# Kernel optimization log

Hardware: AMD Instinct MI355X
Metric: run time of the kernel (lower is better)

Reference implementation:

```python
import jax, jax.numpy as jnp
import numpy as np
import math

EPS = 1e-5

def make_coords(H, W):
    # Faithful port of generate_coordinates (batch-independent; channels 8,9 stay zero).
    cy = H / 2.0 - 0.5
    cx = W / 2.0 - 0.5
    gx, gy = np.meshgrid(np.arange(H, dtype=np.float32), np.arange(W, dtype=np.float32), indexing='ij')
    two_pi = 2.0 * math.pi
    theta = np.arctan2(gy - cx, gx - cy) % two_pi
    theta = np.round(10000.0 * theta) / 10000.0
    coords = np.zeros((H, W, 18), dtype=np.float32)
    adds = [(1, 1), (1, 0), (1, -1), (0, 1), None, (0, -1), (-1, 1), (-1, 0), (-1, -1)]
    for k, add in enumerate(adds):
        if add is None:
            continue  # center tap offset left at zero (as in source)
        n = k if k < 4 else k - 1
        a = theta + n * (two_pi / 8.0)
        coords[:, :, 2 * k] = np.cos(a) + add[0]
        coords[:, :, 2 * k + 1] = np.sin(a) + add[1]
    return jnp.asarray(coords)

def bilinear_sample(x, py, px):
    # x: [B,C,H,W]; py/px: [H,W] sample coords; zero outside boundaries (torchvision semantics).
    H, W = x.shape[2], x.shape[3]
    y0f = jnp.floor(py); x0f = jnp.floor(px)
    wy1 = py - y0f; wy0 = 1.0 - wy1
    wx1 = px - x0f; wx0 = 1.0 - wx1
    def gather(yf, xf):
        valid = ((yf >= 0) & (yf < H) & (xf >= 0) & (xf < W)).astype(x.dtype)
        yi = jnp.clip(yf, 0, H - 1).astype(jnp.int32)
        xi = jnp.clip(xf, 0, W - 1).astype(jnp.int32)
        return x[:, :, yi, xi] * valid  # [B,C,H,W]
    return (gather(y0f, x0f) * (wy0 * wx0) + gather(y0f, x0f + 1) * (wy0 * wx1)
            + gather(y0f + 1, x0f) * (wy1 * wx0) + gather(y0f + 1, x0f + 1) * (wy1 * wx1))

def deform_conv(x, coords, weight, pad=1):
    # x: [B,Cin,H,W]; coords: [H,W,18] with (dy,dx) pairs per 3x3 tap; weight: [Cout,Cin,3,3]; no bias.
    B, C, H, W = x.shape
    ys = jnp.arange(H, dtype=x.dtype)[:, None]
    xs = jnp.arange(W, dtype=x.dtype)[None, :]
    out = jnp.zeros((B, weight.shape[0], H, W), x.dtype)
    for k in range(9):  # fixed 3x3 taps
        kh, kw = k // 3, k % 3
        py = ys - pad + kh + coords[..., 2 * k]
        px = xs - pad + kw + coords[..., 2 * k + 1]
        samp = bilinear_sample(x, py, px)
        out = out + jnp.einsum('bchw,oc->bohw', samp, weight[:, :, kh, kw])
    return out

def bn_relu(x, gamma, beta):
    # BatchNorm2d in training mode (batch statistics, biased variance) + ReLU.
    mu = x.mean(axis=(0, 2, 3), keepdims=True)
    var = ((x - mu) ** 2).mean(axis=(0, 2, 3), keepdims=True)
    xn = (x - mu) * jax.lax.rsqrt(var + EPS)
    return jax.nn.relu(xn * gamma[None, :, None, None] + beta[None, :, None, None])

def maxpool2(x):
    B, C, H, W = x.shape
    return x.reshape(B, C, H // 2, 2, W // 2, 2).max(axis=(3, 5))

def setup_inputs() -> dict:
    key = jax.random.key(0)
    ks = jax.random.split(key, 16)
    B = 1024
    def conv_w(k, co, ci):
        return jax.random.normal(k, (co, ci, 3, 3), jnp.float32) * (1.0 / np.sqrt(ci * 9))
    inp = {
        'x': jax.random.normal(ks[0], (B, 1, 32, 32), jnp.float32),
        'w11': conv_w(ks[1], 32, 1),  'g11': jnp.ones(32),  'b11': jnp.zeros(32),
        'w12': conv_w(ks[2], 32, 32), 'g12': jnp.ones(32),  'b12': jnp.zeros(32),
        'w21': conv_w(ks[3], 64, 32), 'g21': jnp.ones(64),  'b21': jnp.zeros(64),
        'w22': conv_w(ks[4], 64, 64), 'g22': jnp.ones(64),  'b22': jnp.zeros(64),
        'w31': conv_w(ks[5], 128, 64),  'g31': jnp.ones(128), 'b31': jnp.zeros(128),
        'w32': conv_w(ks[6], 128, 128), 'g32': jnp.ones(128), 'b32': jnp.zeros(128),
        'fcw': jax.random.normal(ks[7], (10, 128), jnp.float32) * (1.0 / np.sqrt(128)),
        'fcb': jnp.zeros(10),
        'c32': make_coords(32, 32),
        'c16': make_coords(16, 16),
        'c8': make_coords(8, 8),
    }
    return inp

def reference(x, w11, g11, b11, w12, g12, b12, w21, g21, b21, w22, g22, b22,
              w31, g31, b31, w32, g32, b32, fcw, fcb, c32, c16, c8):
    x = bn_relu(deform_conv(x, c32, w11), g11, b11)
    x = bn_relu(deform_conv(x, c32, w12), g12, b12)
    x = maxpool2(x)                      # [B,32,16,16]
    x = bn_relu(deform_conv(x, c16, w21), g21, b21)
    x = bn_relu(deform_conv(x, c16, w22), g22, b22)
    x = maxpool2(x)                      # [B,64,8,8]
    x = bn_relu(deform_conv(x, c8, w31), g31, b31)
    x = bn_relu(deform_conv(x, c8, w32), g32, b32)
    x = x.mean(axis=(2, 3))              # AvgPool2d(8) over full 8x8 -> [B,128]
    return x @ fcw.T + fcb               # [B,10]
```

## Files before the change

### kernel.cpp

```cpp
#include <hip/hip_runtime.h>
#include <math.h>


#define BATCH 1024
typedef unsigned short u16;
typedef unsigned int uint;
typedef __attribute__((ext_vector_type(8))) short short8;
typedef __attribute__((ext_vector_type(4))) float f32x4;
typedef __attribute__((ext_vector_type(2))) float f32x2;

__device__ __forceinline__ float b2f(u16 v) {
    return __uint_as_float(((uint)v) << 16);
}
__device__ __forceinline__ float4 b2f4(ushort4 v) {
    return make_float4(b2f(v.x), b2f(v.y), b2f(v.z), b2f(v.w));
}
__device__ __forceinline__ u16 f2b(float f) {
    uint u = __float_as_uint(f);
    return (u16)((u + 0x7FFFu + ((u >> 16) & 1u)) >> 16);
}
__device__ __forceinline__ float ldf(const void* p, long long i, int isbf) {
    return isbf ? b2f(((const u16*)p)[i]) : ((const float*)p)[i];
}
__device__ __forceinline__ f32x2 upk(uint u) {
    f32x2 r;
    r.x = __uint_as_float(u << 16);
    r.y = __uint_as_float(u & 0xFFFF0000u);
    return r;
}

struct Ptrs { const void* p[24]; int sz[24]; };

__global__ __launch_bounds__(256) void probe_dtype(Ptrs P, int* __restrict__ flags)
{
    int t = blockIdx.x;
    bool ones = (t == 2 || t == 5 || t == 8 || t == 11 || t == 14 || t == 17);
    bool inh  = (t == 3 || t == 6 || t == 9 || t == 12 || t == 15 || t == 18 || t == 20);
    if (inh) return;
    const u16* q = (const u16*)P.p[t];
    if (ones) {
        if (threadIdx.x == 0) {
            uint w0 = *(const uint*)q;
            flags[t] = (w0 == 0x3F803F80u) ? 1 : 0;
        }
        return;
    }
    int n = P.sz[t]; if (n > 4096) n = 4096;
    __shared__ int cnt;
    if (threadIdx.x == 0) cnt = 0;
    __syncthreads();
    int local = 0;
    for (int i = threadIdx.x; i < n; i += 256) {
        uint e = (q[i] >> 7) & 0xFFu;
        if (!(e == 0u || (e >= 100u && e <= 140u))) local++;
    }
    atomicAdd(&cnt, local);
    __syncthreads();
    if (threadIdx.x == 0) flags[t] = (cnt * 8 > n) ? 0 : 1;
}

__global__ void fixup_flags(int* __restrict__ flags)
{
    if (threadIdx.x == 0) {
        flags[3] = flags[2];  flags[6] = flags[5];  flags[9] = flags[8];
        flags[12] = flags[11]; flags[15] = flags[14]; flags[18] = flags[17];
        flags[20] = flags[19];
    }
}

__device__ void table_body(const void* coords, int H, int W,
                           int* tIdx, float* tW, int fcd, int i)
{
    int HW = H * W;
    if (i >= HW * 9) return;
    int p = i / 9, k = i % 9;
    int h = p / W, w = p % W;
    int kh = k / 3, kw = k % 3;
    float py = (float)(h - 1 + kh) + ldf(coords, p * 18 + 2 * k, fcd);
    float px = (float)(w - 1 + kw) + ldf(coords, p * 18 + 2 * k + 1, fcd);
    float y0f = floorf(py), x0f = floorf(px);
    float wy1 = py - y0f, wy0 = 1.0f - wy1;
    float wx1 = px - x0f, wx0 = 1.0f - wx1;
    int y0 = (int)y0f, x0 = (int)x0f;
#pragma unroll
    for (int j = 0; j < 4; ++j) {
        int dy = j >> 1, dx = j & 1;
        int yy = y0 + dy, xx = x0 + dx;
        bool valid = (yy >= 0) && (yy < H) && (xx >= 0) && (xx < W);
        int yc = min(max(yy, 0), H - 1);
        int xc = min(max(xx, 0), W - 1);
        tIdx[i * 4 + j] = yc * W + xc;
        tW[i * 4 + j] = valid ? (dy ? wy1 : wy0) * (dx ? wx1 : wx0) : 0.0f;
    }
}

__global__ __launch_bounds__(256) void build_tables(
    const void* c32, const void* c16, const void* c8,
    int* tI32, float* tW32, int* tI16, float* tW16, int* tI8, float* tW8,
    const int* __restrict__ flags)
{
    int b = blockIdx.x, t = threadIdx.x;
    if (b < 36)      table_body(c32, 32, 32, tI32, tW32, flags[21], b * 256 + t);
    else if (b < 45) table_body(c16, 16, 16, tI16, tW16, flags[22], (b - 36) * 256 + t);
    else             table_body(c8, 8, 8, tI8, tW8, flags[23], (b - 45) * 256 + t);
}

__global__ __launch_bounds__(256) void transpose_in(
    const void* __restrict__ x, u16* __restrict__ X0, const int* __restrict__ flags)
{
    int fx = flags[0];
    int p = blockIdx.x;
    int t = threadIdx.x;
    ushort4 v;
    v.x = f2b(ldf(x, (long long)(4 * t + 0) * 1024 + p, fx));
    v.y = f2b(ldf(x, (long long)(4 * t + 1) * 1024 + p, fx));
    v.z = f2b(ldf(x, (long long)(4 * t + 2) * 1024 + p, fx));
    v.w = f2b(ldf(x, (long long)(4 * t + 3) * 1024 + p, fx));
    ((ushort4*)(X0 + (size_t)p * BATCH))[t] = v;
}

__device__ void wb_body(const void* W, u16* Wb, int Cout, int Cin, int fw, int i)
{
    int c8 = i & 7;
    int r = i >> 3;
    int m = r % Cout;
    int r2 = r / Cout;
    int noct = Cin >> 3;
    int oc = r2 % noct;
    int k = r2 / noct;
    int c = oc * 8 + c8;
    Wb[i] = f2b(ldf(W, (long long)m * Cin * 9 + c * 9 + k, fw));
}

__global__ __launch_bounds__(256) void prep_all(
    const void* w11, const void* w12, const void* w21, const void* w22,
    const void* w31, const void* w32,
    float* w11p, u16* wb12, u16* wb21, u16* wb22, u16* wb31, u16* wb32,
    const int* __restrict__ flags)
{
    int i = blockIdx.x * 256 + threadIdx.x;
    if (i < 288) {
        int o = i / 9, k = i % 9;
        w11p[k * 32 + o] = ldf(w11, i, flags[1]);
    } else if (i < 9504)   wb_body(w12, wb12, 32, 32, flags[4], i - 288);
    else if (i < 27936)    wb_body(w21, wb21, 64, 32, flags[7], i - 9504);
    else if (i < 64800)    wb_body(w22, wb22, 64, 64, flags[10], i - 27936);
    else if (i < 138528)   wb_body(w31, wb31, 128, 64, flags[13], i - 64800);
    else if (i < 285984)   wb_body(w32, wb32, 128, 128, flags[16], i - 138528);
}

__global__ __launch_bounds__(256) void conv_l11(
    const u16* __restrict__ X0, const float* __restrict__ W2,
    u16* __restrict__ Y, const int* __restrict__ tIdx, const float* __restrict__ tW)
{
    const int id = blockIdx.x;
    const int p = id >> 1;
    const int oBase = (id & 1) * 16;
    const int b4 = threadIdx.x;
    const ushort4* Xu = (const ushort4*)X0;

    float4 acc[16];
#pragma unroll
    for (int o = 0; o < 16; ++o) acc[o] = make_float4(0.f, 0.f, 0.f, 0.f);

#pragma unroll
    for (int k = 0; k < 9; ++k) {
        float4 s = make_float4(0.f, 0.f, 0.f, 0.f);
#pragma unroll
        for (int j = 0; j < 4; ++j) {
            float wgt = tW[p * 36 + k * 4 + j];
            int pix = tIdx[p * 36 + k * 4 + j];
            float4 v = b2f4(Xu[pix * 256 + b4]);
            s.x = fmaf(wgt, v.x, s.x); s.y = fmaf(wgt, v.y, s.y);
            s.z = fmaf(wgt, v.z, s.z); s.w = fmaf(wgt, v.w, s.w);
        }
#pragma unroll
        for (int o = 0; o < 16; ++o) {
            float wv = W2[k * 32 + oBase + o];
            acc[o].x = fmaf(wv, s.x, acc[o].x); acc[o].y = fmaf(wv, s.y, acc[o].y);
            acc[o].z = fmaf(wv, s.z, acc[o].z); acc[o].w = fmaf(wv, s.w, acc[o].w);
        }
    }
#pragma unroll
    for (int bb = 0; bb < 4; ++bb) {
        u16 h[16];
#pragma unroll
        for (int o = 0; o < 16; ++o) h[o] = f2b((&acc[o].x)[bb]);
        uint4 pk;
        pk.x = (uint)h[0] | ((uint)h[1] << 16);
        pk.y = (uint)h[2] | ((uint)h[3] << 16);
        pk.z = (uint)h[4] | ((uint)h[5] << 16);
        pk.w = (uint)h[6] | ((uint)h[7] << 16);
        uint4 pk2;
        pk2.x = (uint)h[8] | ((uint)h[9] << 16);
        pk2.y = (uint)h[10] | ((uint)h[11] << 16);
        pk2.z = (uint)h[12] | ((uint)h[13] << 16);
        pk2.w = (uint)h[14] | ((uint)h[15] << 16);
        size_t base = ((size_t)p * 1024 + 4 * b4 + bb) * 32 + oBase;
        *(uint4*)(Y + base) = pk;
        *(uint4*)(Y + base + 8) = pk2;
    }
}

template<int MF, int NF>
__global__ __launch_bounds__(256) void conv_mfma(
    const u16* __restrict__ X, const u16* __restrict__ Wb,
    u16* __restrict__ Y,
    const int* __restrict__ tIdx, const float* __restrict__ tW,
    int Cin, int Cout, int HW, int pshift)
{
    const int tid = threadIdx.x;
    const int wid = tid >> 6;
    const int lane = tid & 63;
    const int quad = lane >> 4;
    const int l16 = lane & 15;

    const int pper = HW >> 3;
    const int xcd = blockIdx.x & 7;
    const int lid = blockIdx.x >> 3;
    const int p = xcd * pper + (lid & (pper - 1));
    const int yq = lid >> pshift;

    const int nb = yq * (4 * NF * 16);
    const int wn = wid * (NF * 16);

    const int noct = Cin >> 3;
    const size_t pixstride = (size_t)1024 * Cin;

    int roff[NF];
#pragma unroll
    for (int nf = 0; nf < NF; ++nf)
        roff[nf] = (nb + wn + nf * 16 + l16) * Cin + quad * 8;

    f32x4 acc[MF][NF];
#pragma unroll
    for (int mf = 0; mf < MF; ++mf)
#pragma unroll
        for (int nf = 0; nf < NF; ++nf)
            acc[mf][nf] = (f32x4){0.f, 0.f, 0.f, 0.f};

    const int nc = Cin >> 5;
    for (int k = 0; k < 9; ++k) {
        int pix[4]; f32x2 ww[4];
#pragma unroll
        for (int j = 0; j < 4; ++j) {
            pix[j] = __builtin_amdgcn_readfirstlane(tIdx[p * 36 + k * 4 + j]);
            float w = __uint_as_float(__builtin_amdgcn_readfirstlane(
                __float_as_uint(tW[p * 36 + k * 4 + j])));
            ww[j].x = w; ww[j].y = w;
        }
        const u16* xb0 = X + (size_t)pix[0] * pixstride;
        const u16* xb1 = X + (size_t)pix[1] * pixstride;
        const u16* xb2 = X + (size_t)pix[2] * pixstride;
        const u16* xb3 = X + (size_t)pix[3] * pixstride;

        for (int cc = 0; cc < nc; ++cc) {
            const int coff = cc << 5;
            short8 bf[NF];
#pragma unroll
            for (int nf = 0; nf < NF; ++nf) {
                int ro = roff[nf] + coff;
                uint4 v0 = *(const uint4*)(xb0 + ro);
                uint4 v1 = *(const uint4*)(xb1 + ro);
                uint4 v2 = *(const uint4*)(xb2 + ro);
                uint4 v3 = *(const uint4*)(xb3 + ro);
                const uint* a0 = &v0.x; const uint* a1 = &v1.x;
                const uint* a2 = &v2.x; const uint* a3 = &v3.x;
                union { short8 s; uint4 u; } cvt;
                uint o[4];
#pragma unroll
                for (int i = 0; i < 4; ++i) {
                    f32x2 a = upk(a0[i]) * ww[0];
                    a = upk(a1[i]) * ww[1] + a;
                    a = upk(a2[i]) * ww[2] + a;
                    a = upk(a3[i]) * ww[3] + a;
                    o[i] = __builtin_amdgcn_perm(
                        __float_as_uint(a.y) + 0x8000u,
                        __float_as_uint(a.x) + 0x8000u, 0x07060302u);
                }
                cvt.u.x = o[0]; cvt.u.y = o[1]; cvt.u.z = o[2]; cvt.u.w = o[3];
                bf[nf] = cvt.s;
            }
            const u16* wk = Wb + ((size_t)(k * noct + (cc << 2) + quad) * Cout + l16) * 8;
#pragma unroll
            for (int mf = 0; mf < MF; ++mf) {
                const short8 af = *(const short8*)(wk + (size_t)mf * 16 * 8);
#pragma unroll
                for (int nf = 0; nf < NF; ++nf)
                    acc[mf][nf] = __builtin_amdgcn_mfma_f32_16x16x32_bf16(
                        af, bf[nf], acc[mf][nf], 0, 0, 0);
            }
        }
    }

#pragma unroll
    for (int mf = 0; mf < MF; ++mf) {
        int cout0 = mf * 16 + quad * 4;
#pragma unroll
        for (int nf = 0; nf < NF; ++nf) {
            int b = nb + wn + nf * 16 + l16;
            ushort4 pk;
            pk.x = f2b(acc[mf][nf][0]);
            pk.y = f2b(acc[mf][nf][1]);
            pk.z = f2b(acc[mf][nf][2]);
            pk.w = f2b(acc[mf][nf][3]);
            *(ushort4*)(Y + ((size_t)p * 1024 + b) * Cout + cout0) = pk;
        }
    }
}

__global__ __launch_bounds__(256) void bn_stats2(
    const u16* __restrict__ Y, float* __restrict__ stats, int Cin, long long NPB)
{
    const int stride = Cin >> 3;
    const int RPI = 256 / stride;
    const int t = threadIdx.x;
    const int cg = t % stride;
    const int r = t / stride;
    const int lane = t & 63;
    const int wid = t >> 6;

    float s[8], q[8];
#pragma unroll
    for (int j = 0; j < 8; ++j) { s[j] = 0.f; q[j] = 0.f; }

    for (long long row0 = (long long)blockIdx.x * RPI; row0 < NPB;
         row0 += (long long)gridDim.x * RPI) {
        long long row = row0 + r;
        if (row >= NPB) continue;
        uint4 v = *(const uint4*)(Y + row * Cin + cg * 8);
        uint ua[4] = {v.x, v.y, v.z, v.w};
#pragma unroll
        for (int jj = 0; jj < 4; ++jj) {
            float lo = __uint_as_float(ua[jj] << 16);
            float hi = __uint_as_float(ua[jj] & 0xFFFF0000u);
            s[2 * jj] += lo;     q[2 * jj] += lo * lo;
            s[2 * jj + 1] += hi; q[2 * jj + 1] += hi * hi;
        }
    }
    for (int off = 32; off >= stride; off >>= 1) {
#pragma unroll
        for (int j = 0; j < 8; ++j) {
            s[j] += __shfl_down(s[j], off);
            q[j] += __shfl_down(q[j], off);
        }
    }
    __shared__ float rs[4][128], rq[4][128];
    if (lane < stride) {
#pragma unroll
        for (int j = 0; j < 8; ++j) {
            rs[wid][lane * 8 + j] = s[j];
            rq[wid][lane * 8 + j] = q[j];
        }
    }
    __syncthreads();
    if (t < Cin) {
        float S = rs[0][t] + rs[1][t] + rs[2][t] + rs[3][t];
        float Q = rq[0][t] + rq[1][t] + rq[2][t] + rq[3][t];
        atomicAdd(&stats[2 * t], S);
        atomicAdd(&stats[2 * t + 1], Q);
    }
}

__global__ __launch_bounds__(256) void bn_apply2(
    u16* __restrict__ Y, const float* __restrict__ stats,
    const void* __restrict__ gamma, const void* __restrict__ beta,
    int Cin, float invN, long long total8,
    const int* __restrict__ flags, int gslot, int bslot)
{
    __shared__ float sSC[128], sSH[128];
    int fg = flags[gslot], fb = flags[bslot];
    if (threadIdx.x < Cin) {
        int c = threadIdx.x;
        float mean = stats[2 * c] * invN;
        float var = stats[2 * c + 1] * invN - mean * mean;
        float sc = ldf(gamma, c, fg) * rsqrtf(var + 1e-5f);
        sSC[c] = sc;
        sSH[c] = ldf(beta, c, fb) - mean * sc;
    }
    __syncthreads();
    const int stride = Cin >> 3;
    for (long long i = (long long)blockIdx.x * 256 + threadIdx.x; i < total8;
         i += (long long)gridDim.x * 256) {
        int cg = (int)(i % stride);
        uint4* ptr = (uint4*)(Y + i * 8);
        uint4 v = *ptr;
        uint ua[4] = {v.x, v.y, v.z, v.w};
#pragma unroll
        for (int jj = 0; jj < 4; ++jj) {
            int c = cg * 8 + 2 * jj;
            float lo = __uint_as_float(ua[jj] << 16);
            float hi = __uint_as_float(ua[jj] & 0xFFFF0000u);
            lo = fmaxf(fmaf(lo, sSC[c], sSH[c]), 0.f);
            hi = fmaxf(fmaf(hi, sSC[c + 1], sSH[c + 1]), 0.f);
            ua[jj] = ((uint)f2b(hi) << 16) | (uint)f2b(lo);
        }
        v.x = ua[0]; v.y = ua[1]; v.z = ua[2]; v.w = ua[3];
        *ptr = v;
    }
}

__global__ __launch_bounds__(256) void pool_bn(
    const u16* __restrict__ A, u16* __restrict__ P,
    const float* __restrict__ stats,
    const void* __restrict__ gamma, const void* __restrict__ beta,
    const int* __restrict__ flags, int gslot, int bslot,
    int H2, int W2, int C, float invN, long long total)
{
    __shared__ float sSC[128], sSH[128];
    if (threadIdx.x < C) {
        int c = threadIdx.x;
        float mean = stats[2 * c] * invN;
        float var = stats[2 * c + 1] * invN - mean * mean;
        float sc = ldf(gamma, c, flags[gslot]) * rsqrtf(var + 1e-5f);
        sSC[c] = sc;
        sSH[c] = ldf(beta, c, flags[bslot]) - mean * sc;
    }
    __syncthreads();
    long long i = (long long)blockIdx.x * 256 + threadIdx.x;
    if (i >= total) return;
    int cgn = C >> 3;
    int cg = (int)(i % cgn);
    long long row = i / cgn;
    int b = (int)(row & 1023);
    int p2 = (int)(row >> 10);
    int h2 = p2 / W2, w2 = p2 % W2;
    int W = 2 * W2;
    int p00 = (2 * h2) * W + 2 * w2;
    const u16* base = A + (size_t)cg * 8;
    uint4 va = *(const uint4*)(base + ((size_t)(p00)*1024 + b) * C);
    uint4 vb = *(const uint4*)(base + ((size_t)(p00 + 1) * 1024 + b) * C);
    uint4 vd = *(const uint4*)(base + ((size_t)(p00 + W) * 1024 + b) * C);
    uint4 ve = *(const uint4*)(base + ((size_t)(p00 + W + 1) * 1024 + b) * C);
    uint ra[4] = {va.x, va.y, va.z, va.w};
    uint rb[4] = {vb.x, vb.y, vb.z, vb.w};
    uint rd[4] = {vd.x, vd.y, vd.z, vd.w};
    uint re[4] = {ve.x, ve.y, ve.z, ve.w};
    uint ro[4];
#pragma unroll
    for (int j = 0; j < 4; ++j) {
        int c = cg * 8 + 2 * j;
        float lo = fmaxf(fmaxf(__uint_as_float(ra[j] << 16), __uint_as_float(rb[j] << 16)),
                         fmaxf(__uint_as_float(rd[j] << 16), __uint_as_float(re[j] << 16)));
        float hi = fmaxf(fmaxf(__uint_as_float(ra[j] & 0xFFFF0000u), __uint_as_float(rb[j] & 0xFFFF0000u)),
                         fmaxf(__uint_as_float(rd[j] & 0xFFFF0000u), __uint_as_float(re[j] & 0xFFFF0000u)));
        lo = fmaxf(fmaf(lo, sSC[c], sSH[c]), 0.f);
        hi = fmaxf(fmaf(hi, sSC[c + 1], sSH[c + 1]), 0.f);
        ro[j] = ((uint)f2b(hi) << 16) | (uint)f2b(lo);
    }
    uint4 m; m.x = ro[0]; m.y = ro[1]; m.z = ro[2]; m.w = ro[3];
    *(uint4*)(P + ((size_t)p2 * 1024 + b) * C + cg * 8) = m;
}

__global__ __launch_bounds__(256) void avg_bn(
    const u16* __restrict__ A, float* __restrict__ M,
    const float* __restrict__ stats,
    const void* __restrict__ gamma, const void* __restrict__ beta,
    const int* __restrict__ flags, int gslot, int bslot, float invN)
{
    __shared__ float sSC[128], sSH[128];
    if (threadIdx.x < 128) {
        int c = threadIdx.x;
        float mean = stats[2 * c] * invN;
        float var = stats[2 * c + 1] * invN - mean * mean;
        float sc = ldf(gamma, c, flags[gslot]) * rsqrtf(var + 1e-5f);
        sSC[c] = sc;
        sSH[c] = ldf(beta, c, flags[bslot]) - mean * sc;
    }
    __syncthreads();
    int i = blockIdx.x * 256 + threadIdx.x;
    int b = i >> 4, cg = i & 15;
    float s[8];
#pragma unroll
    for (int j = 0; j < 8; ++j) s[j] = 0.f;
    for (int p = 0; p < 64; ++p) {
        uint4 v = *(const uint4*)(A + ((size_t)p * 1024 + b) * 128 + cg * 8);
        uint ua[4] = {v.x, v.y, v.z, v.w};
#pragma unroll
        for (int jj = 0; jj < 4; ++jj) {
            int c = cg * 8 + 2 * jj;
            float lo = __uint_as_float(ua[jj] << 16);
            float hi = __uint_as_float(ua[jj] & 0xFFFF0000u);
            s[2 * jj] += fmaxf(fmaf(lo, sSC[c], sSH[c]), 0.f);
            s[2 * jj + 1] += fmaxf(fmaf(hi, sSC[c + 1], sSH[c + 1]), 0.f);
        }
    }
#pragma unroll
    for (int j = 0; j < 8; ++j) M[(size_t)b * 128 + cg * 8 + j] = s[j] * (1.0f / 64.0f);
}

__global__ __launch_bounds__(256) void fc_naive(
    const float* __restrict__ M, const void* __restrict__ fcw,
    const void* __restrict__ fcb, float* __restrict__ out, int total,
    const int* __restrict__ flags)
{
    int fw = flags[19], fb = flags[20];
    int i = blockIdx.x * 256 + threadIdx.x;
    if (i >= total) return;
    int o = i % 10, b = i / 10;
    float acc = ldf(fcb, o, fb);
    const float* Mb = M + (size_t)b * 128;
    for (int c = 0; c < 128; ++c) acc = fmaf(Mb[c], ldf(fcw, (size_t)o * 128 + c, fw), acc);
    out[i] = acc;
}

__global__ __launch_bounds__(256) void sentinel_k(float* out, int n, float v) {
    int i = blockIdx.x * 256 + threadIdx.x;
    if (i < n) out[i] = v;
}

extern "C" void kernel_launch(void* const* d_in, const int* in_sizes, int n_in,
                              void* d_out, int out_size, void* d_ws, size_t ws_size,
                              hipStream_t stream) {
    float* out = (float*)d_out;

    static const int exp_sizes[24] = {
        1024 * 1024,
        288, 32, 32,   9216, 32, 32,   18432, 64, 64,   36864, 64, 64,
        73728, 128, 128,   147456, 128, 128,
        1280, 10,   18432, 4608, 1152
    };
    float bad = 0.0f;
    if (n_in != 24) bad = 1000.0f;
    else {
        for (int i = 0; i < 24; ++i)
            if (in_sizes[i] != exp_sizes[i]) { bad = 2000.0f + 16.0f * i; break; }
    }
    if (bad != 0.0f) {
        sentinel_k<<<(out_size + 255) / 256, 256, 0, stream>>>(out, out_size, bad);
        return;
    }

    Ptrs P;
    for (int i = 0; i < 24; ++i) { P.p[i] = d_in[i]; P.sz[i] = in_sizes[i]; }

    char* wsb = (char*)d_ws;
    size_t off = 0;
    auto take = [&](size_t bytes) -> void* {
        void* pp = wsb + off;
        off += (bytes + 255) & ~(size_t)255;
        return pp;
    };
    int*   flags = (int*)  take(32 * 4);
    float* stats = (float*)take(6 * 256 * 4);
    int*   tI32  = (int*)  take(1024 * 36 * 4);
    float* tW32  = (float*)take(1024 * 36 * 4);
    int*   tI16  = (int*)  take(256 * 36 * 4);
    float* tW16  = (float*)take(256 * 36 * 4);
    int*   tI8   = (int*)  take(64 * 36 * 4);
    float* tW8   = (float*)take(64 * 36 * 4);
    float* w11p  = (float*)take(32 * 9 * 4);
    u16*   wb12  = (u16*)  take(32 * 32 * 9 * 2);
    u16*   wb21  = (u16*)  take(64 * 32 * 9 * 2);
    u16*   wb22  = (u16*)  take(64 * 64 * 9 * 2);
    u16*   wb31  = (u16*)  take(128 * 64 * 9 * 2);
    u16*   wb32  = (u16*)  take(128 * 128 * 9 * 2);
    u16*   X0    = (u16*)  take((size_t)1024 * BATCH * 2);
    float* M     = (float*)take((size_t)BATCH * 128 * 4);
    u16*   bufA  = (u16*)  take((size_t)32 * 1024 * BATCH * 2);
    u16*   bufB  = (u16*)  take((size_t)32 * 1024 * BATCH * 2);

    if (ws_size < off) {
        sentinel_k<<<(out_size + 255) / 256, 256, 0, stream>>>(out, out_size, 12345.0f);
        return;
    }

    probe_dtype<<<24, 256, 0, stream>>>(P, flags);
    fixup_flags<<<1, 64, 0, stream>>>(flags);
    hipMemsetAsync(stats, 0, 6 * 256 * 4, stream);
    build_tables<<<48, 256, 0, stream>>>(d_in[21], d_in[22], d_in[23],
                                         tI32, tW32, tI16, tW16, tI8, tW8, flags);
    transpose_in<<<1024, 256, 0, stream>>>(d_in[0], X0, flags);
    prep_all<<<1118, 256, 0, stream>>>(d_in[1], d_in[4], d_in[7], d_in[10], d_in[13], d_in[16],
                                       w11p, wb12, wb21, wb22, wb31, wb32, flags);

    float* st0 = stats + 0 * 256;
    float* st1 = stats + 1 * 256;
    float* st2 = stats + 2 * 256;
    float* st3 = stats + 3 * 256;
    float* st4 = stats + 4 * 256;
    float* st5 = stats + 5 * 256;

    conv_l11<<<2048, 256, 0, stream>>>(X0, w11p, bufA, tI32, tW32);
    bn_stats2<<<256, 256, 0, stream>>>(bufA, st0, 32, 1048576LL);
    bn_apply2<<<2048, 256, 0, stream>>>(bufA, st0, d_in[2], d_in[3], 32,
                                        1.0f / 1048576.0f, 4194304LL, flags, 2, 3);
    conv_mfma<2, 4><<<4096, 256, 0, stream>>>(bufA, wb12, bufB, tI32, tW32, 32, 32, 1024, 7);
    bn_stats2<<<256, 256, 0, stream>>>(bufB, st1, 32, 1048576LL);
    pool_bn<<<4096, 256, 0, stream>>>(bufB, bufA, st1, d_in[5], d_in[6], flags, 5, 6,
                                      16, 16, 32, 1.0f / 1048576.0f, 1048576LL);
    conv_mfma<4, 4><<<1024, 256, 0, stream>>>(bufA, wb21, bufB, tI16, tW16, 32, 64, 256, 5);
    bn_stats2<<<256, 256, 0, stream>>>(bufB, st2, 64, 262144LL);
    bn_apply2<<<2048, 256, 0, stream>>>(bufB, st2, d_in[8], d_in[9], 64,
                                        1.0f / 262144.0f, 2097152LL, flags, 8, 9);
    conv_mfma<4, 4><<<1024, 256, 0, stream>>>(bufB, wb22, bufA, tI16, tW16, 64, 64, 256, 5);
    bn_stats2<<<256, 256, 0, stream>>>(bufA, st3, 64, 262144LL);
    pool_bn<<<2048, 256, 0, stream>>>(bufA, bufB, st3, d_in[11], d_in[12], flags, 11, 12,
                                      8, 8, 64, 1.0f / 262144.0f, 524288LL);
    conv_mfma<8, 2><<<512, 256, 0, stream>>>(bufB, wb31, bufA, tI8, tW8, 64, 128, 64, 3);
    bn_stats2<<<256, 256, 0, stream>>>(bufA, st4, 128, 65536LL);
    bn_apply2<<<2048, 256, 0, stream>>>(bufA, st4, d_in[14], d_in[15], 128,
                                        1.0f / 65536.0f, 1048576LL, flags, 14, 15);
    conv_mfma<8, 2><<<512, 256, 0, stream>>>(bufA, wb32, bufB, tI8, tW8, 128, 128, 64, 3);
    bn_stats2<<<256, 256, 0, stream>>>(bufB, st5, 128, 65536LL);
    avg_bn<<<64, 256, 0, stream>>>(bufB, M, st5, d_in[17], d_in[18], flags, 17, 18,
                                   1.0f / 65536.0f);
    fc_naive<<<40, 256, 0, stream>>>(M, d_in[19], d_in[20], out, 10240, flags);
}
```

Baseline: 945.1 us.

## Fuse BN+ReLU into deformable conv input gather and drop bn_apply passes

Removes the three standalone bn_apply2 passes and applies batch-norm scale/shift plus ReLU inside conv_mfma to each gathered bilinear tap before interpolation. This saves a full read-modify-write of the activation tensor per layer. The conv loop order is swapped to channel-chunk outer, tap inner, so per-channel scale/shift are loaded once per chunk. NF is halved with grid doubled for layers 2-3 to raise parallelism. Normalization is now recomputed four times per sample per tap, which adds ALU work in the gather.

```diff
diff --git a/kernel.cpp b/kernel.cpp
--- a/kernel.cpp
+++ b/kernel.cpp
@@ -202,13 +202,29 @@
     }
 }
 
-template<int MF, int NF>
+template<int MF, int NF, int BNORM>
 __global__ __launch_bounds__(256) void conv_mfma(
     const u16* __restrict__ X, const u16* __restrict__ Wb,
     u16* __restrict__ Y,
     const int* __restrict__ tIdx, const float* __restrict__ tW,
-    int Cin, int Cout, int HW, int pshift)
-{
+    int Cin, int Cout, int HW, int pshift,
+    const float* __restrict__ stats, const void* __restrict__ gamma,
+    const void* __restrict__ beta, const int* __restrict__ flags,
+    int gslot, int bslot, float invN)
+{
+    __shared__ float sSC[128], sSH[128];
+    if (BNORM) {
+        if (threadIdx.x < Cin) {
+            int c = threadIdx.x;
+            float mean = stats[2 * c] * invN;
+            float var = stats[2 * c + 1] * invN - mean * mean;
+            float sc = ldf(gamma, c, flags[gslot]) * rsqrtf(var + 1e-5f);
+            sSC[c] = sc;
+            sSH[c] = ldf(beta, c, flags[bslot]) - mean * sc;
+        }
+        __syncthreads();
+    }
+
     const int tid = threadIdx.x;
     const int wid = tid >> 6;
     const int lane = tid & 63;
@@ -240,22 +256,31 @@
             acc[mf][nf] = (f32x4){0.f, 0.f, 0.f, 0.f};
 
     const int nc = Cin >> 5;
-    for (int k = 0; k < 9; ++k) {
-        int pix[4]; f32x2 ww[4];
-#pragma unroll
-        for (int j = 0; j < 4; ++j) {
-            pix[j] = __builtin_amdgcn_readfirstlane(tIdx[p * 36 + k * 4 + j]);
-            float w = __uint_as_float(__builtin_amdgcn_readfirstlane(
-                __float_as_uint(tW[p * 36 + k * 4 + j])));
-            ww[j].x = w; ww[j].y = w;
-        }
-        const u16* xb0 = X + (size_t)pix[0] * pixstride;
-        const u16* xb1 = X + (size_t)pix[1] * pixstride;
-        const u16* xb2 = X + (size_t)pix[2] * pixstride;
-        const u16* xb3 = X + (size_t)pix[3] * pixstride;
-
-        for (int cc = 0; cc < nc; ++cc) {
-            const int coff = cc << 5;
+    for (int cc = 0; cc < nc; ++cc) {
+        const int coff = cc << 5;
+        f32x2 sc2[4], sh2[4];
+        if (BNORM) {
+            int c0 = coff + quad * 8;
+#pragma unroll
+            for (int i = 0; i < 4; ++i) {
+                sc2[i] = *(const f32x2*)(sSC + c0 + 2 * i);
+                sh2[i] = *(const f32x2*)(sSH + c0 + 2 * i);
+            }
+        }
+        for (int k = 0; k < 9; ++k) {
+            int pix[4]; f32x2 ww[4];
+#pragma unroll
+            for (int j = 0; j < 4; ++j) {
+                pix[j] = __builtin_amdgcn_readfirstlane(tIdx[p * 36 + k * 4 + j]);
+                float w = __uint_as_float(__builtin_amdgcn_readfirstlane(
+                    __float_as_uint(tW[p * 36 + k * 4 + j])));
+                ww[j].x = w; ww[j].y = w;
+            }
+            const u16* xb0 = X + (size_t)pix[0] * pixstride;
+            const u16* xb1 = X + (size_t)pix[1] * pixstride;
+            const u16* xb2 = X + (size_t)pix[2] * pixstride;
+            const u16* xb3 = X + (size_t)pix[3] * pixstride;
+
             short8 bf[NF];
 #pragma unroll
             for (int nf = 0; nf < NF; ++nf) {
@@ -270,10 +295,22 @@
                 uint o[4];
 #pragma unroll
                 for (int i = 0; i < 4; ++i) {
-                    f32x2 a = upk(a0[i]) * ww[0];
-                    a = upk(a1[i]) * ww[1] + a;
-                    a = upk(a2[i]) * ww[2] + a;
-                    a = upk(a3[i]) * ww[3] + a;
+                    f32x2 t0 = upk(a0[i]), t1 = upk(a1[i]);
+                    f32x2 t2 = upk(a2[i]), t3 = upk(a3[i]);
+                    if (BNORM) {
+                        t0 = t0 * sc2[i] + sh2[i];
+                        t1 = t1 * sc2[i] + sh2[i];
+                        t2 = t2 * sc2[i] + sh2[i];
+                        t3 = t3 * sc2[i] + sh2[i];
+                        t0.x = fmaxf(t0.x, 0.f); t0.y = fmaxf(t0.y, 0.f);
+                        t1.x = fmaxf(t1.x, 0.f); t1.y = fmaxf(t1.y, 0.f);
+                        t2.x = fmaxf(t2.x, 0.f); t2.y = fmaxf(t2.y, 0.f);
+                        t3.x = fmaxf(t3.x, 0.f); t3.y = fmaxf(t3.y, 0.f);
+                    }
+                    f32x2 a = t0 * ww[0];
+                    a = t1 * ww[1] + a;
+                    a = t2 * ww[2] + a;
+                    a = t3 * ww[3] + a;
                     o[i] = __builtin_amdgcn_perm(
                         __float_as_uint(a.y) + 0x8000u,
                         __float_as_uint(a.x) + 0x8000u, 0x07060302u);
@@ -359,44 +396,6 @@
         float Q = rq[0][t] + rq[1][t] + rq[2][t] + rq[3][t];
         atomicAdd(&stats[2 * t], S);
         atomicAdd(&stats[2 * t + 1], Q);
-    }
-}
-
-__global__ __launch_bounds__(256) void bn_apply2(
-    u16* __restrict__ Y, const float* __restrict__ stats,
-    const void* __restrict__ gamma, const void* __restrict__ beta,
-    int Cin, float invN, long long total8,
-    const int* __restrict__ flags, int gslot, int bslot)
-{
-    __shared__ float sSC[128], sSH[128];
-    int fg = flags[gslot], fb = flags[bslot];
-    if (threadIdx.x < Cin) {
-        int c = threadIdx.x;
-        float mean = stats[2 * c] * invN;
-        float var = stats[2 * c + 1] * invN - mean * mean;
-        float sc = ldf(gamma, c, fg) * rsqrtf(var + 1e-5f);
-        sSC[c] = sc;
-        sSH[c] = ldf(beta, c, fb) - mean * sc;
-    }
-    __syncthreads();
-    const int stride = Cin >> 3;
-    for (long long i = (long long)blockIdx.x * 256 + threadIdx.x; i < total8;
-         i += (long long)gridDim.x * 256) {
-        int cg = (int)(i % stride);
-        uint4* ptr = (uint4*)(Y + i * 8);
-        uint4 v = *ptr;
-        uint ua[4] = {v.x, v.y, v.z, v.w};
-#pragma unroll
-        for (int jj = 0; jj < 4; ++jj) {
-            int c = cg * 8 + 2 * jj;
-            float lo = __uint_as_float(ua[jj] << 16);
-            float hi = __uint_as_float(ua[jj] & 0xFFFF0000u);
-            lo = fmaxf(fmaf(lo, sSC[c], sSH[c]), 0.f);
-            hi = fmaxf(fmaf(hi, sSC[c + 1], sSH[c + 1]), 0.f);
-            ua[jj] = ((uint)f2b(hi) << 16) | (uint)f2b(lo);
-        }
-        v.x = ua[0]; v.y = ua[1]; v.z = ua[2]; v.w = ua[3];
-        *ptr = v;
     }
 }
 
@@ -583,25 +582,24 @@
 
     conv_l11<<<2048, 256, 0, stream>>>(X0, w11p, bufA, tI32, tW32);
     bn_stats2<<<256, 256, 0, stream>>>(bufA, st0, 32, 1048576LL);
-    bn_apply2<<<2048, 256, 0, stream>>>(bufA, st0, d_in[2], d_in[3], 32,
-                                        1.0f / 1048576.0f, 4194304LL, flags, 2, 3);
-    conv_mfma<2, 4><<<4096, 256, 0, stream>>>(bufA, wb12, bufB, tI32, tW32, 32, 32, 1024, 7);
+    conv_mfma<2, 4, 1><<<4096, 256, 0, stream>>>(bufA, wb12, bufB, tI32, tW32, 32, 32, 1024, 7,
+                                                 st0, d_in[2], d_in[3], flags, 2, 3, 1.0f / 1048576.0f);
     bn_stats2<<<256, 256, 0, stream>>>(bufB, st1, 32, 1048576LL);
     pool_bn<<<4096, 256, 0, stream>>>(bufB, bufA, st1, d_in[5], d_in[6], flags, 5, 6,
                                       16, 16, 32, 1.0f / 1048576.0f, 1048576LL);
-    conv_mfma<4, 4><<<1024, 256, 0, stream>>>(bufA, wb21, bufB, tI16, tW16, 32, 64, 256, 5);
+    conv_mfma<4, 2, 0><<<2048, 256, 0, stream>>>(bufA, wb21, bufB, tI16, tW16, 32, 64, 256, 5,
+                                                 st0, d_in[2], d_in[3], flags, 2, 3, 0.f);
     bn_stats2<<<256, 256, 0, stream>>>(bufB, st2, 64, 262144LL);
-    bn_apply2<<<2048, 256, 0, stream>>>(bufB, st2, d_in[8], d_in[9], 64,
-                                        1.0f / 262144.0f, 2097152LL, flags, 8, 9);
-    conv_mfma<4, 4><<<1024, 256, 0, stream>>>(bufB, wb22, bufA, tI16, tW16, 64, 64, 256, 5);
+    conv_mfma<4, 2, 1><<<2048, 256, 0, stream>>>(bufB, wb22, bufA, tI16, tW16, 64, 64, 256, 5,
+                                                 st2, d_in[8], d_in[9], flags, 8, 9, 1.0f / 262144.0f);
     bn_stats2<<<256, 256, 0, stream>>>(bufA, st3, 64, 262144LL);
     pool_bn<<<2048, 256, 0, stream>>>(bufA, bufB, st3, d_in[11], d_in[12], flags, 11, 12,
                                       8, 8, 64, 1.0f / 262144.0f, 524288LL);
-    conv_mfma<8, 2><<<512, 256, 0, stream>>>(bufB, wb31, bufA, tI8, tW8, 64, 128, 64, 3);
+    conv_mfma<8, 1, 0><<<1024, 256, 0, stream>>>(bufB, wb31, bufA, tI8, tW8, 64, 128, 64, 3,
+                                                 st0, d_in[2], d_in[3], flags, 2, 3, 0.f);
     bn_stats2<<<256, 256, 0, stream>>>(bufA, st4, 128, 65536LL);
-    bn_apply2<<<2048, 256, 0, stream>>>(bufA, st4, d_in[14], d_in[15], 128,
-                                        1.0f / 65536.0f, 1048576LL, flags, 14, 15);
-    conv_mfma<8, 2><<<512, 256, 0, stream>>>(bufA, wb32, bufB, tI8, tW8, 128, 128, 64, 3);
+    conv_mfma<8, 1, 1><<<1024, 256, 0, stream>>>(bufA, wb32, bufB, tI8, tW8, 128, 128, 64, 3,
+                                                 st4, d_in[14], d_in[15], flags, 14, 15, 1.0f / 65536.0f);
     bn_stats2<<<256, 256, 0, stream>>>(bufB, st5, 128, 65536LL);
     avg_bn<<<64, 256, 0, stream>>>(bufB, M, st5, d_in[17], d_in[18], flags, 17, 18,
                                    1.0f / 65536.0f);
```

Measured after the change: 879.2 us. -7.0%, faster.

## Fold bilinear tap weights into per-position conv weights instead of blending activations

Applied to the files above, without the earlier changes.

Precomputes, in chunks of output positions, effective bf16 weights equal to each conv weight times its bilinear tap weight, so the MFMA kernel streams the 36 raw gathered pixels directly as B operands. This removes the per-element unpack/FMA/repack blending of four neighbours before each MFMA, at the cost of four times more MFMA work, extra prep kernels and launches per chunk, and a large per-position weight buffer in workspace. Tile shapes change for the later layers, and tap tables are staged in shared memory, including in the first-layer kernel. Rounding changes because products are rounded to bf16 before accumulation.

```diff
diff --git a/kernel.cpp b/kernel.cpp
--- a/kernel.cpp
+++ b/kernel.cpp
@@ -149,12 +149,49 @@
     else if (i < 285984)   wb_body(w32, wb32, 128, 128, flags[16], i - 138528);
 }
 
+__global__ __launch_bounds__(256) void prep_weff(
+    const u16* __restrict__ Wb, const float* __restrict__ tW,
+    u16* __restrict__ Weff, int Cout, int noct, int p0, long long total8)
+{
+    long long j = (long long)blockIdx.x * 256 + threadIdx.x;
+    if (j >= total8) return;
+    long long r = j;
+    int m = (int)(r % Cout); r /= Cout;
+    int oc = (int)(r % noct); r /= noct;
+    int kj = (int)(r % 36); r /= 36;
+    int pl = (int)r;
+    int k = kj >> 2;
+    float w = tW[(size_t)(p0 + pl) * 36 + kj];
+    union { short8 s; uint4 u; } in, outv;
+    in.s = *(const short8*)(Wb + ((size_t)(k * noct + oc) * Cout + m) * 8);
+    uint a[4] = {in.u.x, in.u.y, in.u.z, in.u.w};
+    f32x2 w2; w2.x = w; w2.y = w;
+    uint o[4];
+#pragma unroll
+    for (int i = 0; i < 4; ++i) {
+        f32x2 t = upk(a[i]) * w2;
+        o[i] = __builtin_amdgcn_perm(
+            __float_as_uint(t.y) + 0x8000u,
+            __float_as_uint(t.x) + 0x8000u, 0x07060302u);
+    }
+    outv.u.x = o[0]; outv.u.y = o[1]; outv.u.z = o[2]; outv.u.w = o[3];
+    *(short8*)(Weff + j * 8) = outv.s;
+}
+
 __global__ __launch_bounds__(256) void conv_l11(
     const u16* __restrict__ X0, const float* __restrict__ W2,
     u16* __restrict__ Y, const int* __restrict__ tIdx, const float* __restrict__ tW)
 {
+    __shared__ int sIdx[36];
+    __shared__ float sWt[36];
     const int id = blockIdx.x;
     const int p = id >> 1;
+    if (threadIdx.x < 36) {
+        sIdx[threadIdx.x] = tIdx[p * 36 + threadIdx.x];
+        sWt[threadIdx.x] = tW[p * 36 + threadIdx.x];
+    }
+    __syncthreads();
+
     const int oBase = (id & 1) * 16;
     const int b4 = threadIdx.x;
     const ushort4* Xu = (const ushort4*)X0;
@@ -168,8 +205,8 @@
         float4 s = make_float4(0.f, 0.f, 0.f, 0.f);
 #pragma unroll
         for (int j = 0; j < 4; ++j) {
-            float wgt = tW[p * 36 + k * 4 + j];
-            int pix = tIdx[p * 36 + k * 4 + j];
+            float wgt = sWt[k * 4 + j];
+            int pix = sIdx[k * 4 + j];
             float4 v = b2f4(Xu[pix * 256 + b4]);
             s.x = fmaf(wgt, v.x, s.x); s.y = fmaf(wgt, v.y, s.y);
             s.z = fmaf(wgt, v.z, s.z); s.w = fmaf(wgt, v.w, s.w);
@@ -203,24 +240,27 @@
 }
 
 template<int MF, int NF>
-__global__ __launch_bounds__(256) void conv_mfma(
-    const u16* __restrict__ X, const u16* __restrict__ Wb,
-    u16* __restrict__ Y,
-    const int* __restrict__ tIdx, const float* __restrict__ tW,
-    int Cin, int Cout, int HW, int pshift)
-{
+__global__ __launch_bounds__(256) void conv_mfma2(
+    const u16* __restrict__ X, const u16* __restrict__ Weff,
+    u16* __restrict__ Y, const int* __restrict__ tIdx,
+    int Cin, int Cout, int p0, int pper)
+{
+    __shared__ int sIdx[36];
+    const int xcd = blockIdx.x & 7;
+    const int lid = blockIdx.x >> 3;
+    const int pl = xcd * pper + (lid % pper);
+    const int yq = lid / pper;
+    const int p = p0 + pl;
+
+    if (threadIdx.x < 36) sIdx[threadIdx.x] = tIdx[p * 36 + threadIdx.x];
+    __syncthreads();
+
     const int tid = threadIdx.x;
     const int wid = tid >> 6;
     const int lane = tid & 63;
     const int quad = lane >> 4;
     const int l16 = lane & 15;
 
-    const int pper = HW >> 3;
-    const int xcd = blockIdx.x & 7;
-    const int lid = blockIdx.x >> 3;
-    const int p = xcd * pper + (lid & (pper - 1));
-    const int yq = lid >> pshift;
-
     const int nb = yq * (4 * NF * 16);
     const int wn = wid * (NF * 16);
 
@@ -240,48 +280,17 @@
             acc[mf][nf] = (f32x4){0.f, 0.f, 0.f, 0.f};
 
     const int nc = Cin >> 5;
-    for (int k = 0; k < 9; ++k) {
-        int pix[4]; f32x2 ww[4];
-#pragma unroll
-        for (int j = 0; j < 4; ++j) {
-            pix[j] = __builtin_amdgcn_readfirstlane(tIdx[p * 36 + k * 4 + j]);
-            float w = __uint_as_float(__builtin_amdgcn_readfirstlane(
-                __float_as_uint(tW[p * 36 + k * 4 + j])));
-            ww[j].x = w; ww[j].y = w;
-        }
-        const u16* xb0 = X + (size_t)pix[0] * pixstride;
-        const u16* xb1 = X + (size_t)pix[1] * pixstride;
-        const u16* xb2 = X + (size_t)pix[2] * pixstride;
-        const u16* xb3 = X + (size_t)pix[3] * pixstride;
-
-        for (int cc = 0; cc < nc; ++cc) {
-            const int coff = cc << 5;
+    for (int cc = 0; cc < nc; ++cc) {
+        const int coff = cc << 5;
+        for (int kj = 0; kj < 36; ++kj) {
+            int pix = __builtin_amdgcn_readfirstlane(sIdx[kj]);
+            const u16* xb = X + (size_t)pix * pixstride + coff;
             short8 bf[NF];
 #pragma unroll
-            for (int nf = 0; nf < NF; ++nf) {
-                int ro = roff[nf] + coff;
-                uint4 v0 = *(const uint4*)(xb0 + ro);
-                uint4 v1 = *(const uint4*)(xb1 + ro);
-                uint4 v2 = *(const uint4*)(xb2 + ro);
-                uint4 v3 = *(const uint4*)(xb3 + ro);
-                const uint* a0 = &v0.x; const uint* a1 = &v1.x;
-                const uint* a2 = &v2.x; const uint* a3 = &v3.x;
-                union { short8 s; uint4 u; } cvt;
-                uint o[4];
-#pragma unroll
-                for (int i = 0; i < 4; ++i) {
-                    f32x2 a = upk(a0[i]) * ww[0];
-                    a = upk(a1[i]) * ww[1] + a;
-                    a = upk(a2[i]) * ww[2] + a;
-                    a = upk(a3[i]) * ww[3] + a;
-                    o[i] = __builtin_amdgcn_perm(
-                        __float_as_uint(a.y) + 0x8000u,
-                        __float_as_uint(a.x) + 0x8000u, 0x07060302u);
-                }
-                cvt.u.x = o[0]; cvt.u.y = o[1]; cvt.u.z = o[2]; cvt.u.w = o[3];
-                bf[nf] = cvt.s;
-            }
-            const u16* wk = Wb + ((size_t)(k * noct + (cc << 2) + quad) * Cout + l16) * 8;
+            for (int nf = 0; nf < NF; ++nf)
+                bf[nf] = *(const short8*)(xb + roff[nf]);
+            const u16* wk = Weff +
+                (((size_t)(pl * 36 + kj) * noct + (cc << 2) + quad) * Cout + l16) * 8;
 #pragma unroll
             for (int mf = 0; mf < MF; ++mf) {
                 const short8 af = *(const short8*)(wk + (size_t)mf * 16 * 8);
@@ -560,10 +569,21 @@
     u16*   bufA  = (u16*)  take((size_t)32 * 1024 * BATCH * 2);
     u16*   bufB  = (u16*)  take((size_t)32 * 1024 * BATCH * 2);
 
-    if (ws_size < off) {
+    if (ws_size < off + (11u << 20)) {
         sentinel_k<<<(out_size + 255) / 256, 256, 0, stream>>>(out, out_size, 12345.0f);
         return;
     }
+    u16* weff = (u16*)(wsb + off);
+    size_t availB = ws_size - off;
+    if (availB > (80u << 20)) availB = (80u << 20);
+
+    auto pcCalc = [&](int HW, size_t bytesPerPos) -> int {
+        size_t maxpc = availB / bytesPerPos;
+        int lim = (maxpc < (size_t)HW) ? (int)maxpc : HW;
+        int pc = 8;
+        while (pc * 2 <= lim) pc <<= 1;
+        return pc;
+    };
 
     probe_dtype<<<24, 256, 0, stream>>>(P, flags);
     fixup_flags<<<1, 64, 0, stream>>>(flags);
@@ -585,23 +605,63 @@
     bn_stats2<<<256, 256, 0, stream>>>(bufA, st0, 32, 1048576LL);
     bn_apply2<<<2048, 256, 0, stream>>>(bufA, st0, d_in[2], d_in[3], 32,
                                         1.0f / 1048576.0f, 4194304LL, flags, 2, 3);
-    conv_mfma<2, 4><<<4096, 256, 0, stream>>>(bufA, wb12, bufB, tI32, tW32, 32, 32, 1024, 7);
+
+    {
+        int pc = pcCalc(1024, 36 * 32 * 32 * 2);
+        for (int q0 = 0; q0 < 1024; q0 += pc) {
+            long long t8 = (long long)pc * 36 * 4 * 32;
+            prep_weff<<<(int)((t8 + 255) / 256), 256, 0, stream>>>(wb12, tW32, weff, 32, 4, q0, t8);
+            conv_mfma2<2, 4><<<pc * 4, 256, 0, stream>>>(bufA, weff, bufB, tI32, 32, 32, q0, pc / 8);
+        }
+    }
     bn_stats2<<<256, 256, 0, stream>>>(bufB, st1, 32, 1048576LL);
     pool_bn<<<4096, 256, 0, stream>>>(bufB, bufA, st1, d_in[5], d_in[6], flags, 5, 6,
                                       16, 16, 32, 1.0f / 1048576.0f, 1048576LL);
-    conv_mfma<4, 4><<<1024, 256, 0, stream>>>(bufA, wb21, bufB, tI16, tW16, 32, 64, 256, 5);
+
+    {
+        int pc = pcCalc(256, 36 * 32 * 64 * 2);
+        for (int q0 = 0; q0 < 256; q0 += pc) {
+            long long t8 = (long long)pc * 36 * 4 * 64;
+            prep_weff<<<(int)((t8 + 255) / 256), 256, 0, stream>>>(wb21, tW16, weff, 64, 4, q0, t8);
+            conv_mfma2<4, 2><<<pc * 8, 256, 0, stream>>>(bufA, weff, bufB, tI16, 32, 64, q0, pc / 8);
+        }
+    }
     bn_stats2<<<256, 256, 0, stream>>>(bufB, st2, 64, 262144LL);
     bn_apply2<<<2048, 256, 0, stream>>>(bufB, st2, d_in[8], d_in[9], 64,
                                         1.0f / 262144.0f, 2097152LL, flags, 8, 9);
-    conv_mfma<4, 4><<<1024, 256, 0, stream>>>(bufB, wb22, bufA, tI16, tW16, 64, 64, 256, 5);
+
+    {
+        int pc = pcCalc(256, 36 * 64 * 64 * 2);
+        for (int q0 = 0; q0 < 256; q0 += pc) {
+            long long t8 = (long long)pc * 36 * 8 * 64;
+            prep_weff<<<(int)((t8 + 255) / 256), 256, 0, stream>>>(wb22, tW16, weff, 64, 8, q0, t8);
+            conv_mfma2<4, 2><<<pc * 8, 256, 0, stream>>>(bufB, weff, bufA, tI16, 64, 64, q0, pc / 8);
+        }
+    }
     bn_stats2<<<256, 256, 0, stream>>>(bufA, st3, 64, 262144LL);
     pool_bn<<<2048, 256, 0, stream>>>(bufA, bufB, st3, d_in[11], d_in[12], flags, 11, 12,
                                       8, 8, 64, 1.0f / 262144.0f, 524288LL);
-    conv_mfma<8, 2><<<512, 256, 0, stream>>>(bufB, wb31, bufA, tI8, tW8, 64, 128, 64, 3);
+
+    {
+        int pc = pcCalc(64, 36 * 64 * 128 * 2);
+        for (int q0 = 0; q0 < 64; q0 += pc) {
+            long long t8 = (long long)pc * 36 * 8 * 128;
+            prep_weff<<<(int)((t8 + 255) / 256), 256, 0, stream>>>(wb31, tW8, weff, 128, 8, q0, t8);
+            conv_mfma2<8, 1><<<pc * 16, 256, 0, stream>>>(bufB, weff, bufA, tI8, 64, 128, q0, pc / 8);
+        }
+    }
     bn_stats2<<<256, 256, 0, stream>>>(bufA, st4, 128, 65536LL);
     bn_apply2<<<2048, 256, 0, stream>>>(bufA, st4, d_in[14], d_in[15], 128,
                                         1.0f / 65536.0f, 1048576LL, flags, 14, 15);
-    conv_mfma<8, 2><<<512, 256, 0, stream>>>(bufA, wb32, bufB, tI8, tW8, 128, 128, 64, 3);
+
+    {
+        int pc = pcCalc(64, 36 * 128 * 128 * 2);
+        for (int q0 = 0; q0 < 64; q0 += pc) {
+            long long t8 = (long long)pc * 36 * 16 * 128;
+            prep_weff<<<(int)((t8 + 255) / 256), 256, 0, stream>>>(wb32, tW8, weff, 128, 16, q0, t8);
+            conv_mfma2<8, 1><<<pc * 16, 256, 0, stream>>>(bufA, weff, bufB, tI8, 128, 128, q0, pc / 8);
+        }
+    }
     bn_stats2<<<256, 256, 0, stream>>>(bufB, st5, 128, 65536LL);
     avg_bn<<<64, 256, 0, stream>>>(bufB, M, st5, d_in[17], d_in[18], flags, 17, 18,
                                    1.0f / 65536.0f);
```

New measurement: 1.262 ms. 33.5% more time.
